# Optimization experiments

Measured on AMD Instinct MI355X. Metric: run time of the kernel, lower is better.

Reference implementation:

```python
import jax, jax.numpy as jnp
import numpy as np

EPS = 1e-5  # torch.nn.LayerNorm default
NUM_HEADS = 8


def _layernorm(x, g, b):
    mu = jnp.mean(x, axis=-1, keepdims=True)
    var = jnp.mean((x - mu) ** 2, axis=-1, keepdims=True)
    return (x - mu) * jax.lax.rsqrt(var + EPS) * g + b


def setup_inputs() -> dict:
    key = jax.random.key(0)
    ks = jax.random.split(key, 8)
    B, S, D = 4, 2048, 512
    scale = 0.02
    return {
        'x': jax.random.normal(ks[0], (B, S, D), dtype=jnp.float32),
        'gene_types': jax.random.randint(ks[1], (B, S), 0, 2),
        'tf_g': jnp.ones((D,), jnp.float32), 'tf_b': jnp.zeros((D,), jnp.float32),
        'tg_g': jnp.ones((D,), jnp.float32), 'tg_b': jnp.zeros((D,), jnp.float32),
        'in_proj_w': jax.random.normal(ks[2], (3 * D, D), dtype=jnp.float32) * scale,
        'in_proj_b': jnp.zeros((3 * D,), jnp.float32),
        'out_proj_w': jax.random.normal(ks[3], (D, D), dtype=jnp.float32) * scale,
        'out_proj_b': jnp.zeros((D,), jnp.float32),
        'w1': jax.random.normal(ks[4], (D // 2, D), dtype=jnp.float32) * scale,
        'b1': jnp.zeros((D // 2,), jnp.float32),
        'w2': jax.random.normal(ks[5], (1, D // 2), dtype=jnp.float32) * scale,
        'b2': jnp.zeros((1,), jnp.float32),
    }


def reference(x, gene_types, tf_g, tf_b, tg_g, tg_b,
              in_proj_w, in_proj_b, out_proj_w, out_proj_b,
              w1, b1, w2, b2):
    B, S, D = x.shape
    H = NUM_HEADS
    HD = D // H
    # --- vectorized per-token conditional LayerNorm (gene_type 0 -> tf, 1 -> target, else passthrough) ---
    gt = gene_types[..., None]
    xn = jnp.where(gt == 0, _layernorm(x, tf_g, tf_b),
                   jnp.where(gt == 1, _layernorm(x, tg_g, tg_b), x))
    # --- multi-head self-attention (torch MultiheadAttention, batch_first) ---
    qkv = xn @ in_proj_w.T + in_proj_b            # [B,S,3D]
    q, k, v = jnp.split(qkv, 3, axis=-1)
    to_heads = lambda t: t.reshape(B, S, H, HD).transpose(0, 2, 1, 3)  # [B,H,S,HD]
    q, k, v = to_heads(q), to_heads(k), to_heads(v)
    scores = jnp.einsum('bhqd,bhkd->bhqk', q, k) / jnp.sqrt(jnp.float32(HD))
    attn = jax.nn.softmax(scores, axis=-1)
    o = jnp.einsum('bhqk,bhkd->bhqd', attn, v)
    o = o.transpose(0, 2, 1, 3).reshape(B, S, D)
    o = o @ out_proj_w.T + out_proj_b
    xr = xn + o                                    # residual
    # --- regulatory strength gate: Linear -> SiLU -> Linear -> Sigmoid ---
    h = jax.nn.silu(xr @ w1.T + b1)                # [B,S,D/2]
    strength = jax.nn.sigmoid(h @ w2.T + b2)       # [B,S,1]
    return xr * strength
```

## Files before the change

kernel.cpp:

```cpp
#include <hip/hip_runtime.h>

typedef __bf16 bf16;
typedef __bf16 bf16x4_t __attribute__((ext_vector_type(4)));
typedef __bf16 bf16x8_t __attribute__((ext_vector_type(8)));
typedef float f32x4_t __attribute__((ext_vector_type(4)));

#define MFMA16(a, b, c) __builtin_amdgcn_mfma_f32_16x16x32_bf16(a, b, c, 0, 0, 0)

__global__ __launch_bounds__(256) void castln_k(const float* __restrict__ Wqkv,
                                                const float* __restrict__ Wout,
                                                const float* __restrict__ W1,
                                                bf16* __restrict__ wq,
                                                bf16* __restrict__ wo,
                                                bf16* __restrict__ w1b,
                                                const float* __restrict__ x,
                                                const int* __restrict__ gt,
                                                const float* __restrict__ tfg,
                                                const float* __restrict__ tfb,
                                                const float* __restrict__ tgg,
                                                const float* __restrict__ tgb,
                                                bf16* __restrict__ xn) {
    if (blockIdx.x < 4608) {
        int i = blockIdx.x * 256 + threadIdx.x;
        if (i < 786432) wq[i] = (bf16)Wqkv[i];
        else if (i < 1048576) wo[i - 786432] = (bf16)Wout[i - 786432];
        else if (i < 1179648) w1b[i - 1048576] = (bf16)W1[i - 1048576];
        return;
    }
    int wid = threadIdx.x >> 6, lane = threadIdx.x & 63;
    int t = (blockIdx.x - 4608) * 4 + wid;
    const float4* xr = (const float4*)(x + (size_t)t * 512);
    float4 a = xr[lane * 2], b = xr[lane * 2 + 1];
    float s = (a.x + a.y) + (a.z + a.w) + (b.x + b.y) + (b.z + b.w);
    float sq = a.x * a.x + a.y * a.y + a.z * a.z + a.w * a.w +
               b.x * b.x + b.y * b.y + b.z * b.z + b.w * b.w;
    for (int m = 1; m < 64; m <<= 1) {
        s += __shfl_xor(s, m, 64);
        sq += __shfl_xor(sq, m, 64);
    }
    float mean = s * (1.f / 512.f);
    float var = fmaxf(sq * (1.f / 512.f) - mean * mean, 0.f);
    float rstd = rsqrtf(var + 1e-5f);
    int g = gt[t];
    float4 o0, o1;
    if (g < 2) {
        const float4* gp = (const float4*)(g ? tgg : tfg);
        const float4* bp = (const float4*)(g ? tgb : tfb);
        float4 g0 = gp[lane * 2], g1 = gp[lane * 2 + 1];
        float4 b0 = bp[lane * 2], b1 = bp[lane * 2 + 1];
        o0.x = (a.x - mean) * rstd * g0.x + b0.x;
        o0.y = (a.y - mean) * rstd * g0.y + b0.y;
        o0.z = (a.z - mean) * rstd * g0.z + b0.z;
        o0.w = (a.w - mean) * rstd * g0.w + b0.w;
        o1.x = (b.x - mean) * rstd * g1.x + b1.x;
        o1.y = (b.y - mean) * rstd * g1.y + b1.y;
        o1.z = (b.z - mean) * rstd * g1.z + b1.z;
        o1.w = (b.w - mean) * rstd * g1.w + b1.w;
    } else {
        o0 = a; o1 = b;
    }
    bf16* xo = xn + (size_t)t * 512 + lane * 8;
    bf16x4_t p0, p1;
    p0[0] = (bf16)o0.x; p0[1] = (bf16)o0.y; p0[2] = (bf16)o0.z; p0[3] = (bf16)o0.w;
    p1[0] = (bf16)o1.x; p1[1] = (bf16)o1.y; p1[2] = (bf16)o1.z; p1[3] = (bf16)o1.w;
    *(bf16x4_t*)xo = p0;
    *(bf16x4_t*)(xo + 4) = p1;
}

__global__ __launch_bounds__(256) void gemmqkv_k(const bf16* __restrict__ A,
                                                 const bf16* __restrict__ B,
                                                 const float* __restrict__ bias,
                                                 bf16* __restrict__ q,
                                                 bf16* __restrict__ kk,
                                                 bf16* __restrict__ vv) {
    int m0 = blockIdx.x * 128, n0 = blockIdx.y * 128;
    int tid = threadIdx.x;
    int lane = tid & 63, w = tid >> 6;
    int quad = lane >> 4, l15 = lane & 15;
    int wm = (w >> 1) * 64, wn = (w & 1) * 64;
    __shared__ bf16 As[128 * 72];
    __shared__ bf16 Bs[128 * 72];
    f32x4_t acc[4][4] = {};
    int srow = tid >> 3, ssub = tid & 7;
    const bf16* Ab = A + (size_t)(m0 + srow) * 512 + ssub * 8;
    const bf16* Bb = B + (size_t)(n0 + srow) * 512 + ssub * 8;
    uint4 pa[4], pb[4];
    auto gload = [&](int s) {
        int k0 = s * 64;
#pragma unroll
        for (int i = 0; i < 4; ++i) {
            pa[i] = *(const uint4*)(Ab + (size_t)(i * 32) * 512 + k0);
            pb[i] = *(const uint4*)(Bb + (size_t)(i * 32) * 512 + k0);
        }
    };
    auto sstore = [&]() {
#pragma unroll
        for (int i = 0; i < 4; ++i) {
            *(uint4*)&As[(i * 32 + srow) * 72 + ssub * 8] = pa[i];
            *(uint4*)&Bs[(i * 32 + srow) * 72 + ssub * 8] = pb[i];
        }
    };
    gload(0);
    sstore();
    for (int s = 0; s < 8; ++s) {
        __syncthreads();
        if (s < 7) gload(s + 1);
#pragma unroll
        for (int ks = 0; ks < 2; ++ks) {
            bf16x8_t af[4], bfr[4];
            int koff = ks * 32 + quad * 8;
#pragma unroll
            for (int mt = 0; mt < 4; ++mt)
                af[mt] = *(const bf16x8_t*)&As[(wm + mt * 16 + l15) * 72 + koff];
#pragma unroll
            for (int nt = 0; nt < 4; ++nt)
                bfr[nt] = *(const bf16x8_t*)&Bs[(wn + nt * 16 + l15) * 72 + koff];
#pragma unroll
            for (int mt = 0; mt < 4; ++mt)
#pragma unroll
                for (int nt = 0; nt < 4; ++nt)
                    acc[mt][nt] = MFMA16(af[mt], bfr[nt], acc[mt][nt]);
        }
        __syncthreads();
        if (s < 7) sstore();
    }
#pragma unroll
    for (int mt = 0; mt < 4; ++mt) {
#pragma unroll
        for (int nt = 0; nt < 4; ++nt) {
            int gcol = n0 + wn + nt * 16 + l15;
            float bcol = bias[gcol];
#pragma unroll
            for (int r = 0; r < 4; ++r) {
                int grow = m0 + wm + mt * 16 + quad * 4 + r;
                float v = acc[mt][nt][r] + bcol;
                int which = gcol >> 9;
                int d = gcol & 511;
                int hh = d >> 6, hd = d & 63;
                int b = grow >> 11, ssi = grow & 2047;
                size_t bh = (size_t)(b * 8 + hh);
                size_t idx = (bh * 2048 + ssi) * 64 + hd;
                if (which == 0) {
                    q[idx] = (bf16)(v * 0.180336880111f);
                } else if (which == 1) {
                    kk[idx] = (bf16)v;
                } else {
                    vv[idx] = (bf16)v;
                }
            }
        }
    }
}

__global__ __launch_bounds__(256) void vtrans_k(const bf16* __restrict__ v,
                                                bf16* __restrict__ vt) {
    int bh = blockIdx.y;
    int s0 = blockIdx.x * 64;
    __shared__ bf16 Ls[64][72];
    int tid = threadIdx.x;
    int row = tid >> 2, seg = tid & 3;
    const bf16* vb = v + ((size_t)bh * 2048 + s0 + row) * 64 + seg * 16;
    *(uint4*)&Ls[row][seg * 16] = *(const uint4*)vb;
    *(uint4*)&Ls[row][seg * 16 + 8] = *(const uint4*)(vb + 8);
    __syncthreads();
    bf16 tmp[16];
#pragma unroll
    for (int i = 0; i < 16; ++i) tmp[i] = Ls[seg * 16 + i][row];
    bf16* dst = vt + ((size_t)bh * 64 + row) * 2048 + s0 + seg * 16;
    *(uint4*)dst = *(uint4*)&tmp[0];
    *(uint4*)(dst + 8) = *(uint4*)&tmp[8];
}

__global__ __launch_bounds__(256) void attn_k(const bf16* __restrict__ q,
                                              const bf16* __restrict__ k,
                                              const bf16* __restrict__ vt,
                                              bf16* __restrict__ pO,
                                              float* __restrict__ pL) {
    int bh = blockIdx.y;
    int q0 = blockIdx.x * 128;
    int sz = blockIdx.z;
    int kt0 = sz * 16;
    int tid = threadIdx.x;
    int lane = tid & 63, w = tid >> 6;
    int quad = lane >> 4, l15 = lane & 15;
    __shared__ bf16 Ks[64 * 72];
    __shared__ bf16 Vs[64 * 72];
    __shared__ bf16 Ps[128 * 72];
    const bf16* qb = q + (size_t)bh * 2048 * 64;
    const bf16* kb = k + (size_t)bh * 2048 * 64;
    const bf16* vb = vt + (size_t)bh * 64 * 2048;
    bf16x8_t qf[2][2];
#pragma unroll
    for (int mt = 0; mt < 2; ++mt)
#pragma unroll
        for (int ks = 0; ks < 2; ++ks)
            qf[mt][ks] = *(const bf16x8_t*)(qb + (size_t)(q0 + w * 32 + mt * 16 + l15) * 64 + ks * 32 + quad * 8);
    bf16x8_t ones8;
#pragma unroll
    for (int i = 0; i < 8; ++i) ones8[i] = (bf16)1.0f;
    f32x4_t oacc[2][4] = {};
    f32x4_t lacc[2] = {};
    int srow = tid >> 3, ssub = tid & 7;
    uint4 pk[2], pw[2];
    auto gload = [&](int kt) {
        int kbase = kt * 64;
#pragma unroll
        for (int i = 0; i < 2; ++i) {
            int row = i * 32 + srow;
            pk[i] = *(const uint4*)(kb + (size_t)(kbase + row) * 64 + ssub * 8);
            pw[i] = *(const uint4*)(vb + (size_t)row * 2048 + kbase + ssub * 8);
        }
    };
    auto sstore = [&]() {
#pragma unroll
        for (int i = 0; i < 2; ++i) {
            int row = i * 32 + srow;
            *(uint4*)&Ks[row * 72 + ssub * 8] = pk[i];
            *(uint4*)&Vs[row * 72 + ssub * 8] = pw[i];
        }
    };
    gload(kt0);
    for (int kt = kt0; kt < kt0 + 16; ++kt) {
        __syncthreads();
        sstore();
        __syncthreads();
        if (kt + 1 < kt0 + 16) gload(kt + 1);
        f32x4_t sacc[2][4] = {};
#pragma unroll
        for (int ks = 0; ks < 2; ++ks) {
            int koff = ks * 32 + quad * 8;
            bf16x8_t kf[4];
#pragma unroll
            for (int nt = 0; nt < 4; ++nt)
                kf[nt] = *(const bf16x8_t*)&Ks[(nt * 16 + l15) * 72 + koff];
#pragma unroll
            for (int mt = 0; mt < 2; ++mt)
#pragma unroll
                for (int nt = 0; nt < 4; ++nt)
                    sacc[mt][nt] = MFMA16(qf[mt][ks], kf[nt], sacc[mt][nt]);
        }
#pragma unroll
        for (int mt = 0; mt < 2; ++mt)
#pragma unroll
            for (int nt = 0; nt < 4; ++nt)
#pragma unroll
                for (int r = 0; r < 4; ++r)
                    Ps[(w * 32 + mt * 16 + quad * 4 + r) * 72 + nt * 16 + l15] = (bf16)exp2f(sacc[mt][nt][r]);
#pragma unroll
        for (int ks = 0; ks < 2; ++ks) {
            int koff = ks * 32 + quad * 8;
            bf16x8_t pf[2], vf[4];
#pragma unroll
            for (int mt = 0; mt < 2; ++mt)
                pf[mt] = *(const bf16x8_t*)&Ps[(w * 32 + mt * 16 + l15) * 72 + koff];
#pragma unroll
            for (int nt = 0; nt < 4; ++nt)
                vf[nt] = *(const bf16x8_t*)&Vs[(nt * 16 + l15) * 72 + koff];
#pragma unroll
            for (int mt = 0; mt < 2; ++mt) {
#pragma unroll
                for (int nt = 0; nt < 4; ++nt)
                    oacc[mt][nt] = MFMA16(pf[mt], vf[nt], oacc[mt][nt]);
                lacc[mt] = MFMA16(pf[mt], ones8, lacc[mt]);
            }
        }
    }
    size_t obase = ((size_t)(sz * 32 + bh) * 2048 + q0);
#pragma unroll
    for (int mt = 0; mt < 2; ++mt)
#pragma unroll
        for (int r = 0; r < 4; ++r) {
            int row = w * 32 + mt * 16 + quad * 4 + r;
#pragma unroll
            for (int nt = 0; nt < 4; ++nt)
                pO[(obase + row) * 64 + nt * 16 + l15] = (bf16)oacc[mt][nt][r];
            if (l15 == 0) pL[obase + row] = lacc[mt][r];
        }
}

__global__ __launch_bounds__(256) void gemmo_k(const bf16* __restrict__ pO,
                                               const float* __restrict__ pL,
                                               const bf16* __restrict__ B,
                                               const float* __restrict__ bias,
                                               const bf16* __restrict__ xn,
                                               bf16* __restrict__ xrb,
                                               float* __restrict__ xrf) {
    int m0 = blockIdx.x * 128, n0 = blockIdx.y * 128;
    int tid = threadIdx.x;
    int lane = tid & 63, w = tid >> 6;
    int quad = lane >> 4, l15 = lane & 15;
    int wm = (w >> 1) * 64, wn = (w & 1) * 64;
    __shared__ bf16 As[128 * 72];
    __shared__ bf16 Bs[128 * 72];
    f32x4_t acc[4][4] = {};
    int srow = tid >> 3, ssub = tid & 7;
    const bf16* Bb = B + (size_t)(n0 + srow) * 512 + ssub * 8;
    bf16x8_t pa[4];
    uint4 pb[4];
    auto gload = [&](int s) {
        int k0 = s * 64;
#pragma unroll
        for (int i = 0; i < 4; ++i) {
            int t = m0 + i * 32 + srow;
            int b = t >> 11, ssi = t & 2047;
            size_t r0 = ((size_t)(b * 8 + s)) * 2048 + ssi;
            size_t r1 = ((size_t)(32 + b * 8 + s)) * 2048 + ssi;
            float inv = 1.f / (pL[r0] + pL[r1]);
            bf16x8_t a0 = *(const bf16x8_t*)(pO + r0 * 64 + ssub * 8);
            bf16x8_t a1 = *(const bf16x8_t*)(pO + r1 * 64 + ssub * 8);
            bf16x8_t c;
#pragma unroll
            for (int j = 0; j < 8; ++j) c[j] = (bf16)(((float)a0[j] + (float)a1[j]) * inv);
            pa[i] = c;
            pb[i] = *(const uint4*)(Bb + (size_t)(i * 32) * 512 + k0);
        }
    };
    auto sstore = [&]() {
#pragma unroll
        for (int i = 0; i < 4; ++i) {
            *(bf16x8_t*)&As[(i * 32 + srow) * 72 + ssub * 8] = pa[i];
            *(uint4*)&Bs[(i * 32 + srow) * 72 + ssub * 8] = pb[i];
        }
    };
    gload(0);
    sstore();
    for (int s = 0; s < 8; ++s) {
        __syncthreads();
        if (s < 7) gload(s + 1);
#pragma unroll
        for (int ks = 0; ks < 2; ++ks) {
            bf16x8_t af[4], bfr[4];
            int koff = ks * 32 + quad * 8;
#pragma unroll
            for (int mt = 0; mt < 4; ++mt)
                af[mt] = *(const bf16x8_t*)&As[(wm + mt * 16 + l15) * 72 + koff];
#pragma unroll
            for (int nt = 0; nt < 4; ++nt)
                bfr[nt] = *(const bf16x8_t*)&Bs[(wn + nt * 16 + l15) * 72 + koff];
#pragma unroll
            for (int mt = 0; mt < 4; ++mt)
#pragma unroll
                for (int nt = 0; nt < 4; ++nt)
                    acc[mt][nt] = MFMA16(af[mt], bfr[nt], acc[mt][nt]);
        }
        __syncthreads();
        if (s < 7) sstore();
    }
#pragma unroll
    for (int mt = 0; mt < 4; ++mt) {
#pragma unroll
        for (int nt = 0; nt < 4; ++nt) {
            int gcol = n0 + wn + nt * 16 + l15;
            float bcol = bias[gcol];
#pragma unroll
            for (int r = 0; r < 4; ++r) {
                int grow = m0 + wm + mt * 16 + quad * 4 + r;
                size_t idx = (size_t)grow * 512 + gcol;
                float xv = acc[mt][nt][r] + bcol + (float)xn[idx];
                xrf[idx] = xv;
                xrb[idx] = (bf16)xv;
            }
        }
    }
}

__global__ __launch_bounds__(256) void mlp_k(const bf16* __restrict__ A,
                                             const bf16* __restrict__ B,
                                             const float* __restrict__ b1,
                                             const float* __restrict__ w2,
                                             const float* __restrict__ b2,
                                             const float* __restrict__ xrf,
                                             float* __restrict__ out) {
    int m0 = blockIdx.x * 32;
    int tid = threadIdx.x;
    int lane = tid & 63, w = tid >> 6;
    int quad = lane >> 4, l15 = lane & 15;
    int wn = w * 64;
    __shared__ bf16 As[32 * 72];
    __shared__ bf16 Bs[256 * 72];
    __shared__ float red[4][32];
    __shared__ float st[32];
    f32x4_t acc[2][4] = {};
    int srow = tid >> 3, ssub = tid & 7;
    uint4 pa, pb[8];
    auto gload = [&](int s) {
        int k0 = s * 64;
        pa = *(const uint4*)(A + (size_t)(m0 + srow) * 512 + ssub * 8 + k0);
#pragma unroll
        for (int i = 0; i < 8; ++i)
            pb[i] = *(const uint4*)(B + (size_t)(i * 32 + srow) * 512 + ssub * 8 + k0);
    };
    auto sstore = [&]() {
        *(uint4*)&As[srow * 72 + ssub * 8] = pa;
#pragma unroll
        for (int i = 0; i < 8; ++i)
            *(uint4*)&Bs[(i * 32 + srow) * 72 + ssub * 8] = pb[i];
    };
    gload(0);
    sstore();
    for (int s = 0; s < 8; ++s) {
        __syncthreads();
        if (s < 7) gload(s + 1);
#pragma unroll
        for (int ks = 0; ks < 2; ++ks) {
            int koff = ks * 32 + quad * 8;
            bf16x8_t af[2], bfr[4];
#pragma unroll
            for (int mt = 0; mt < 2; ++mt)
                af[mt] = *(const bf16x8_t*)&As[(mt * 16 + l15) * 72 + koff];
#pragma unroll
            for (int nt = 0; nt < 4; ++nt)
                bfr[nt] = *(const bf16x8_t*)&Bs[(wn + nt * 16 + l15) * 72 + koff];
#pragma unroll
            for (int mt = 0; mt < 2; ++mt)
#pragma unroll
                for (int nt = 0; nt < 4; ++nt)
                    acc[mt][nt] = MFMA16(af[mt], bfr[nt], acc[mt][nt]);
        }
        __syncthreads();
        if (s < 7) sstore();
    }
    f32x4_t ds[2] = {};
#pragma unroll
    for (int mt = 0; mt < 2; ++mt)
#pragma unroll
        for (int nt = 0; nt < 4; ++nt) {
            int gcol = wn + nt * 16 + l15;
            float bb = b1[gcol], ww = w2[gcol];
#pragma unroll
            for (int r = 0; r < 4; ++r) {
                float v = acc[mt][nt][r] + bb;
                float sv = v / (1.f + __expf(-v));
                ds[mt][r] += sv * ww;
            }
        }
#pragma unroll
    for (int m = 1; m < 16; m <<= 1)
#pragma unroll
        for (int mt = 0; mt < 2; ++mt)
#pragma unroll
            for (int r = 0; r < 4; ++r) ds[mt][r] += __shfl_xor(ds[mt][r], m, 64);
    if (l15 == 0) {
#pragma unroll
        for (int mt = 0; mt < 2; ++mt)
#pragma unroll
            for (int r = 0; r < 4; ++r) red[w][mt * 16 + quad * 4 + r] = ds[mt][r];
    }
    __syncthreads();
    if (tid < 32) {
        float d = red[0][tid] + red[1][tid] + red[2][tid] + red[3][tid] + b2[0];
        st[tid] = 1.f / (1.f + __expf(-d));
    }
    __syncthreads();
    int row = tid >> 3, seg = tid & 7;
    float sr = st[row];
    const float4* x4 = (const float4*)(xrf + (size_t)(m0 + row) * 512);
    float4* o4 = (float4*)(out + (size_t)(m0 + row) * 512);
#pragma unroll
    for (int jj = 0; jj < 16; ++jj) {
        float4 xv = x4[jj * 8 + seg];
        float4 ov;
        ov.x = xv.x * sr; ov.y = xv.y * sr; ov.z = xv.z * sr; ov.w = xv.w * sr;
        o4[jj * 8 + seg] = ov;
    }
}

extern "C" void kernel_launch(void* const* d_in, const int* in_sizes, int n_in,
                              void* d_out, int out_size, void* d_ws, size_t ws_size,
                              hipStream_t stream) {
    const float* x    = (const float*)d_in[0];
    const int*   gt   = (const int*)d_in[1];
    const float* tfg  = (const float*)d_in[2];
    const float* tfb  = (const float*)d_in[3];
    const float* tgg  = (const float*)d_in[4];
    const float* tgb  = (const float*)d_in[5];
    const float* Wqkv = (const float*)d_in[6];
    const float* bqkv = (const float*)d_in[7];
    const float* Wout = (const float*)d_in[8];
    const float* bout = (const float*)d_in[9];
    const float* W1   = (const float*)d_in[10];
    const float* b1   = (const float*)d_in[11];
    const float* w2   = (const float*)d_in[12];
    const float* b2   = (const float*)d_in[13];
    float* out = (float*)d_out;
    char* ws = (char*)d_ws;

    const size_t MB = 1024 * 1024;
    bf16*  wq  = (bf16*)(ws + 0);
    bf16*  wo  = (bf16*)(ws + 1536 * 512 * 2);
    bf16*  w1b = (bf16*)(ws + (1536 + 512) * 512 * 2);
    float* pL  = (float*)(ws + 2304 * 512 * 2);
    bf16*  xn  = (bf16*)(ws + 4 * MB);
    bf16*  q   = (bf16*)(ws + 12 * MB);
    bf16*  xrb = (bf16*)(ws + 12 * MB);
    bf16*  kk  = (bf16*)(ws + 20 * MB);
    bf16*  vv  = (bf16*)(ws + 28 * MB);
    bf16*  vt  = (bf16*)(ws + 36 * MB);
    float* xrf = (float*)(ws + 28 * MB);
    bf16*  pO  = (bf16*)(ws + 44 * MB);

    castln_k<<<6656, 256, 0, stream>>>(Wqkv, Wout, W1, wq, wo, w1b,
                                       x, gt, tfg, tfb, tgg, tgb, xn);
    gemmqkv_k<<<dim3(64, 12), 256, 0, stream>>>(xn, wq, bqkv, q, kk, vv);
    vtrans_k<<<dim3(32, 32), 256, 0, stream>>>(vv, vt);
    attn_k<<<dim3(16, 32, 2), 256, 0, stream>>>(q, kk, vt, pO, pL);
    gemmo_k<<<dim3(64, 4), 256, 0, stream>>>(pO, pL, wo, bout, xn, xrb, xrf);
    mlp_k<<<256, 256, 0, stream>>>(xrb, w1b, b1, w2, b2, xrf, out);
    (void)in_sizes; (void)n_in; (void)out_size; (void)ws_size;
}
```

Baseline: 331.7 us.

## Transpose attention MFMA operands for vectorized P/O stores; drop bf16 residual copy

The attention kernel swaps the MFMA operand order (K·Q and V·P instead of Q·K and P·V), so each lane holds four consecutive key or head-dim values. P tiles and the output partials can then be written as 4-wide bf16 vectors instead of scalar stores. Separately, the output-projection kernel stops writing a bf16 copy of the residual, and the MLP kernel reads the fp32 residual and converts it to bf16 while loading. This saves one global write, at the cost of twice the bytes read in the MLP A-operand load.

```diff
diff --git a/kernel.cpp b/kernel.cpp
--- a/kernel.cpp
+++ b/kernel.cpp
@@ -191,10 +191,10 @@
     const bf16* vb = vt + (size_t)bh * 64 * 2048;
     bf16x8_t qf[2][2];
 #pragma unroll
-    for (int mt = 0; mt < 2; ++mt)
+    for (int qt = 0; qt < 2; ++qt)
 #pragma unroll
         for (int ks = 0; ks < 2; ++ks)
-            qf[mt][ks] = *(const bf16x8_t*)(qb + (size_t)(q0 + w * 32 + mt * 16 + l15) * 64 + ks * 32 + quad * 8);
+            qf[qt][ks] = *(const bf16x8_t*)(qb + (size_t)(q0 + w * 32 + qt * 16 + l15) * 64 + ks * 32 + quad * 8);
     bf16x8_t ones8;
 #pragma unroll
     for (int i = 0; i < 8; ++i) ones8[i] = (bf16)1.0f;
@@ -225,7 +225,7 @@
         sstore();
         __syncthreads();
         if (kt + 1 < kt0 + 16) gload(kt + 1);
-        f32x4_t sacc[2][4] = {};
+        f32x4_t sacc[4][2] = {};
 #pragma unroll
         for (int ks = 0; ks < 2; ++ks) {
             int koff = ks * 32 + quad * 8;
@@ -234,48 +234,52 @@
             for (int nt = 0; nt < 4; ++nt)
                 kf[nt] = *(const bf16x8_t*)&Ks[(nt * 16 + l15) * 72 + koff];
 #pragma unroll
-            for (int mt = 0; mt < 2; ++mt)
-#pragma unroll
-                for (int nt = 0; nt < 4; ++nt)
-                    sacc[mt][nt] = MFMA16(qf[mt][ks], kf[nt], sacc[mt][nt]);
-        }
-#pragma unroll
-        for (int mt = 0; mt < 2; ++mt)
-#pragma unroll
             for (int nt = 0; nt < 4; ++nt)
 #pragma unroll
-                for (int r = 0; r < 4; ++r)
-                    Ps[(w * 32 + mt * 16 + quad * 4 + r) * 72 + nt * 16 + l15] = (bf16)exp2f(sacc[mt][nt][r]);
+                for (int qt = 0; qt < 2; ++qt)
+                    sacc[nt][qt] = MFMA16(kf[nt], qf[qt][ks], sacc[nt][qt]);
+        }
+#pragma unroll
+        for (int nt = 0; nt < 4; ++nt)
+#pragma unroll
+            for (int qt = 0; qt < 2; ++qt) {
+                bf16x4_t pv;
+#pragma unroll
+                for (int r = 0; r < 4; ++r) pv[r] = (bf16)exp2f(sacc[nt][qt][r]);
+                *(bf16x4_t*)&Ps[(w * 32 + qt * 16 + l15) * 72 + nt * 16 + quad * 4] = pv;
+            }
 #pragma unroll
         for (int ks = 0; ks < 2; ++ks) {
             int koff = ks * 32 + quad * 8;
-            bf16x8_t pf[2], vf[4];
-#pragma unroll
-            for (int mt = 0; mt < 2; ++mt)
-                pf[mt] = *(const bf16x8_t*)&Ps[(w * 32 + mt * 16 + l15) * 72 + koff];
-#pragma unroll
-            for (int nt = 0; nt < 4; ++nt)
-                vf[nt] = *(const bf16x8_t*)&Vs[(nt * 16 + l15) * 72 + koff];
-#pragma unroll
-            for (int mt = 0; mt < 2; ++mt) {
-#pragma unroll
-                for (int nt = 0; nt < 4; ++nt)
-                    oacc[mt][nt] = MFMA16(pf[mt], vf[nt], oacc[mt][nt]);
-                lacc[mt] = MFMA16(pf[mt], ones8, lacc[mt]);
+            bf16x8_t vf[4], pf[2];
+#pragma unroll
+            for (int dt = 0; dt < 4; ++dt)
+                vf[dt] = *(const bf16x8_t*)&Vs[(dt * 16 + l15) * 72 + koff];
+#pragma unroll
+            for (int qt = 0; qt < 2; ++qt)
+                pf[qt] = *(const bf16x8_t*)&Ps[(w * 32 + qt * 16 + l15) * 72 + koff];
+#pragma unroll
+            for (int qt = 0; qt < 2; ++qt) {
+#pragma unroll
+                for (int dt = 0; dt < 4; ++dt)
+                    oacc[qt][dt] = MFMA16(vf[dt], pf[qt], oacc[qt][dt]);
+                lacc[qt] = MFMA16(ones8, pf[qt], lacc[qt]);
             }
         }
     }
     size_t obase = ((size_t)(sz * 32 + bh) * 2048 + q0);
 #pragma unroll
-    for (int mt = 0; mt < 2; ++mt)
-#pragma unroll
-        for (int r = 0; r < 4; ++r) {
-            int row = w * 32 + mt * 16 + quad * 4 + r;
-#pragma unroll
-            for (int nt = 0; nt < 4; ++nt)
-                pO[(obase + row) * 64 + nt * 16 + l15] = (bf16)oacc[mt][nt][r];
-            if (l15 == 0) pL[obase + row] = lacc[mt][r];
-        }
+    for (int qt = 0; qt < 2; ++qt) {
+        int qq = w * 32 + qt * 16 + l15;
+#pragma unroll
+        for (int dt = 0; dt < 4; ++dt) {
+            bf16x4_t ov;
+#pragma unroll
+            for (int r = 0; r < 4; ++r) ov[r] = (bf16)oacc[qt][dt][r];
+            *(bf16x4_t*)&pO[(obase + qq) * 64 + dt * 16 + quad * 4] = ov;
+        }
+        if (quad == 0) pL[obase + qq] = lacc[qt][0];
+    }
 }
 
 __global__ __launch_bounds__(256) void gemmo_k(const bf16* __restrict__ pO,
@@ -283,7 +287,6 @@
                                                const bf16* __restrict__ B,
                                                const float* __restrict__ bias,
                                                const bf16* __restrict__ xn,
-                                               bf16* __restrict__ xrb,
                                                float* __restrict__ xrf) {
     int m0 = blockIdx.x * 128, n0 = blockIdx.y * 128;
     int tid = threadIdx.x;
@@ -356,16 +359,13 @@
             for (int r = 0; r < 4; ++r) {
                 int grow = m0 + wm + mt * 16 + quad * 4 + r;
                 size_t idx = (size_t)grow * 512 + gcol;
-                float xv = acc[mt][nt][r] + bcol + (float)xn[idx];
-                xrf[idx] = xv;
-                xrb[idx] = (bf16)xv;
+                xrf[idx] = acc[mt][nt][r] + bcol + (float)xn[idx];
             }
         }
     }
 }
 
-__global__ __launch_bounds__(256) void mlp_k(const bf16* __restrict__ A,
-                                             const bf16* __restrict__ B,
+__global__ __launch_bounds__(256) void mlp_k(const bf16* __restrict__ B,
                                              const float* __restrict__ b1,
                                              const float* __restrict__ w2,
                                              const float* __restrict__ b2,
@@ -382,16 +382,21 @@
     __shared__ float st[32];
     f32x4_t acc[2][4] = {};
     int srow = tid >> 3, ssub = tid & 7;
-    uint4 pa, pb[8];
+    bf16x8_t pa;
+    uint4 pb[8];
     auto gload = [&](int s) {
         int k0 = s * 64;
-        pa = *(const uint4*)(A + (size_t)(m0 + srow) * 512 + ssub * 8 + k0);
+        const float* ar = xrf + (size_t)(m0 + srow) * 512 + ssub * 8 + k0;
+        float4 f0 = *(const float4*)ar;
+        float4 f1 = *(const float4*)(ar + 4);
+        pa[0] = (bf16)f0.x; pa[1] = (bf16)f0.y; pa[2] = (bf16)f0.z; pa[3] = (bf16)f0.w;
+        pa[4] = (bf16)f1.x; pa[5] = (bf16)f1.y; pa[6] = (bf16)f1.z; pa[7] = (bf16)f1.w;
 #pragma unroll
         for (int i = 0; i < 8; ++i)
             pb[i] = *(const uint4*)(B + (size_t)(i * 32 + srow) * 512 + ssub * 8 + k0);
     };
     auto sstore = [&]() {
-        *(uint4*)&As[srow * 72 + ssub * 8] = pa;
+        *(bf16x8_t*)&As[srow * 72 + ssub * 8] = pa;
 #pragma unroll
         for (int i = 0; i < 8; ++i)
             *(uint4*)&Bs[(i * 32 + srow) * 72 + ssub * 8] = pb[i];
@@ -492,11 +497,10 @@
     float* pL  = (float*)(ws + 2304 * 512 * 2);
     bf16*  xn  = (bf16*)(ws + 4 * MB);
     bf16*  q   = (bf16*)(ws + 12 * MB);
-    bf16*  xrb = (bf16*)(ws + 12 * MB);
     bf16*  kk  = (bf16*)(ws + 20 * MB);
+    float* xrf = (float*)(ws + 12 * MB);
     bf16*  vv  = (bf16*)(ws + 28 * MB);
     bf16*  vt  = (bf16*)(ws + 36 * MB);
-    float* xrf = (float*)(ws + 28 * MB);
     bf16*  pO  = (bf16*)(ws + 44 * MB);
 
     castln_k<<<6656, 256, 0, stream>>>(Wqkv, Wout, W1, wq, wo, w1b,
@@ -504,7 +508,7 @@
     gemmqkv_k<<<dim3(64, 12), 256, 0, stream>>>(xn, wq, bqkv, q, kk, vv);
     vtrans_k<<<dim3(32, 32), 256, 0, stream>>>(vv, vt);
     attn_k<<<dim3(16, 32, 2), 256, 0, stream>>>(q, kk, vt, pO, pL);
-    gemmo_k<<<dim3(64, 4), 256, 0, stream>>>(pO, pL, wo, bout, xn, xrb, xrf);
-    mlp_k<<<256, 256, 0, stream>>>(xrb, w1b, b1, w2, b2, xrf, out);
+    gemmo_k<<<dim3(64, 4), 256, 0, stream>>>(pO, pL, wo, bout, xn, xrf);
+    mlp_k<<<256, 256, 0, stream>>>(w1b, b1, w2, b2, xrf, out);
     (void)in_sizes; (void)n_in; (void)out_size; (void)ws_size;
 }
```

Measured after the change: 330.6 us. No clear change (-0.3%).

## Fuse V transpose into QKV GEMM epilogue and widen attention key split

Applied to the files above, without the earlier changes.

The QKV GEMM now writes V directly in transposed layout through a shared-memory staging tile, which removes the separate transpose kernel and its extra round trip of V through memory. The attention kernel is templated on the number of key tiles per split and uses a 4-way split when workspace allows, which gives more blocks and more parallelism, at the cost of more partial results to merge in the output projection. The register prefetch pipeline in attention is dropped in favour of direct global-to-LDS loads. The bf16 copy of the residual is removed, and the MLP instead reads the fp32 residual and casts it on load.

```diff
diff --git a/kernel.cpp b/kernel.cpp
--- a/kernel.cpp
+++ b/kernel.cpp
@@ -72,14 +72,15 @@
                                                  const float* __restrict__ bias,
                                                  bf16* __restrict__ q,
                                                  bf16* __restrict__ kk,
-                                                 bf16* __restrict__ vv) {
+                                                 bf16* __restrict__ vt) {
     int m0 = blockIdx.x * 128, n0 = blockIdx.y * 128;
     int tid = threadIdx.x;
     int lane = tid & 63, w = tid >> 6;
     int quad = lane >> 4, l15 = lane & 15;
     int wm = (w >> 1) * 64, wn = (w & 1) * 64;
-    __shared__ bf16 As[128 * 72];
-    __shared__ bf16 Bs[128 * 72];
+    __shared__ bf16 smem[128 * 144];
+    bf16* As = smem;
+    bf16* Bs = smem + 128 * 72;
     f32x4_t acc[4][4] = {};
     int srow = tid >> 3, ssub = tid & 7;
     const bf16* Ab = A + (size_t)(m0 + srow) * 512 + ssub * 8;
@@ -124,53 +125,57 @@
         __syncthreads();
         if (s < 7) sstore();
     }
-#pragma unroll
-    for (int mt = 0; mt < 4; ++mt) {
-#pragma unroll
-        for (int nt = 0; nt < 4; ++nt) {
-            int gcol = n0 + wn + nt * 16 + l15;
-            float bcol = bias[gcol];
-#pragma unroll
-            for (int r = 0; r < 4; ++r) {
-                int grow = m0 + wm + mt * 16 + quad * 4 + r;
-                float v = acc[mt][nt][r] + bcol;
-                int which = gcol >> 9;
-                int d = gcol & 511;
-                int hh = d >> 6, hd = d & 63;
-                int b = grow >> 11, ssi = grow & 2047;
-                size_t bh = (size_t)(b * 8 + hh);
-                size_t idx = (bh * 2048 + ssi) * 64 + hd;
-                if (which == 0) {
-                    q[idx] = (bf16)(v * 0.180336880111f);
-                } else if (which == 1) {
-                    kk[idx] = (bf16)v;
-                } else {
-                    vv[idx] = (bf16)v;
+    if (blockIdx.y < 8) {
+#pragma unroll
+        for (int mt = 0; mt < 4; ++mt) {
+#pragma unroll
+            for (int nt = 0; nt < 4; ++nt) {
+                int gcol = n0 + wn + nt * 16 + l15;
+                float bcol = bias[gcol];
+#pragma unroll
+                for (int r = 0; r < 4; ++r) {
+                    int grow = m0 + wm + mt * 16 + quad * 4 + r;
+                    float v = acc[mt][nt][r] + bcol;
+                    int d = gcol & 511;
+                    int hh = d >> 6, hd = d & 63;
+                    int b = grow >> 11, ssi = grow & 2047;
+                    size_t idx = (((size_t)(b * 8 + hh)) * 2048 + ssi) * 64 + hd;
+                    if (gcol < 512) q[idx] = (bf16)(v * 0.180336880111f);
+                    else kk[idx] = (bf16)v;
                 }
             }
         }
+    } else {
+        __syncthreads();
+#pragma unroll
+        for (int mt = 0; mt < 4; ++mt)
+#pragma unroll
+            for (int nt = 0; nt < 4; ++nt) {
+                int gcol = n0 + wn + nt * 16 + l15;
+                float bcol = bias[gcol];
+#pragma unroll
+                for (int r = 0; r < 4; ++r) {
+                    int tok = wm + mt * 16 + quad * 4 + r;
+                    smem[tok * 136 + wn + nt * 16 + l15] = (bf16)(acc[mt][nt][r] + bcol);
+                }
+            }
+        __syncthreads();
+        int dl = tid >> 1, seg = tid & 1;
+        int d = (n0 - 1024) + dl;
+        int hh = d >> 6, hd = d & 63;
+        int b = m0 >> 11, ssi0 = m0 & 2047;
+        bf16* dst = vt + ((size_t)(b * 8 + hh) * 64 + hd) * 2048 + ssi0 + seg * 64;
+#pragma unroll
+        for (int u = 0; u < 8; ++u) {
+            bf16 tmp[8];
+#pragma unroll
+            for (int j = 0; j < 8; ++j) tmp[j] = smem[(seg * 64 + u * 8 + j) * 136 + dl];
+            *(uint4*)(dst + u * 8) = *(uint4*)tmp;
+        }
     }
 }
 
-__global__ __launch_bounds__(256) void vtrans_k(const bf16* __restrict__ v,
-                                                bf16* __restrict__ vt) {
-    int bh = blockIdx.y;
-    int s0 = blockIdx.x * 64;
-    __shared__ bf16 Ls[64][72];
-    int tid = threadIdx.x;
-    int row = tid >> 2, seg = tid & 3;
-    const bf16* vb = v + ((size_t)bh * 2048 + s0 + row) * 64 + seg * 16;
-    *(uint4*)&Ls[row][seg * 16] = *(const uint4*)vb;
-    *(uint4*)&Ls[row][seg * 16 + 8] = *(const uint4*)(vb + 8);
-    __syncthreads();
-    bf16 tmp[16];
-#pragma unroll
-    for (int i = 0; i < 16; ++i) tmp[i] = Ls[seg * 16 + i][row];
-    bf16* dst = vt + ((size_t)bh * 64 + row) * 2048 + s0 + seg * 16;
-    *(uint4*)dst = *(uint4*)&tmp[0];
-    *(uint4*)(dst + 8) = *(uint4*)&tmp[8];
-}
-
+template <int TILES>
 __global__ __launch_bounds__(256) void attn_k(const bf16* __restrict__ q,
                                               const bf16* __restrict__ k,
                                               const bf16* __restrict__ vt,
@@ -179,7 +184,6 @@
     int bh = blockIdx.y;
     int q0 = blockIdx.x * 128;
     int sz = blockIdx.z;
-    int kt0 = sz * 16;
     int tid = threadIdx.x;
     int lane = tid & 63, w = tid >> 6;
     int quad = lane >> 4, l15 = lane & 15;
@@ -201,38 +205,23 @@
     f32x4_t oacc[2][4] = {};
     f32x4_t lacc[2] = {};
     int srow = tid >> 3, ssub = tid & 7;
-    uint4 pk[2], pw[2];
-    auto gload = [&](int kt) {
+    for (int kt = sz * TILES; kt < sz * TILES + TILES; ++kt) {
         int kbase = kt * 64;
+        __syncthreads();
 #pragma unroll
         for (int i = 0; i < 2; ++i) {
             int row = i * 32 + srow;
-            pk[i] = *(const uint4*)(kb + (size_t)(kbase + row) * 64 + ssub * 8);
-            pw[i] = *(const uint4*)(vb + (size_t)row * 2048 + kbase + ssub * 8);
-        }
-    };
-    auto sstore = [&]() {
-#pragma unroll
-        for (int i = 0; i < 2; ++i) {
-            int row = i * 32 + srow;
-            *(uint4*)&Ks[row * 72 + ssub * 8] = pk[i];
-            *(uint4*)&Vs[row * 72 + ssub * 8] = pw[i];
-        }
-    };
-    gload(kt0);
-    for (int kt = kt0; kt < kt0 + 16; ++kt) {
-        __syncthreads();
-        sstore();
-        __syncthreads();
-        if (kt + 1 < kt0 + 16) gload(kt + 1);
+            *(uint4*)&Ks[row * 72 + ssub * 8] = *(const uint4*)(kb + (size_t)(kbase + row) * 64 + ssub * 8);
+            *(uint4*)&Vs[row * 72 + ssub * 8] = *(const uint4*)(vb + (size_t)row * 2048 + kbase + ssub * 8);
+        }
+        __syncthreads();
         f32x4_t sacc[2][4] = {};
 #pragma unroll
         for (int ks = 0; ks < 2; ++ks) {
+            bf16x8_t kf[4];
             int koff = ks * 32 + quad * 8;
-            bf16x8_t kf[4];
-#pragma unroll
-            for (int nt = 0; nt < 4; ++nt)
-                kf[nt] = *(const bf16x8_t*)&Ks[(nt * 16 + l15) * 72 + koff];
+#pragma unroll
+            for (int nt = 0; nt < 4; ++nt) kf[nt] = *(const bf16x8_t*)&Ks[(nt * 16 + l15) * 72 + koff];
 #pragma unroll
             for (int mt = 0; mt < 2; ++mt)
 #pragma unroll
@@ -251,11 +240,9 @@
             int koff = ks * 32 + quad * 8;
             bf16x8_t pf[2], vf[4];
 #pragma unroll
-            for (int mt = 0; mt < 2; ++mt)
-                pf[mt] = *(const bf16x8_t*)&Ps[(w * 32 + mt * 16 + l15) * 72 + koff];
-#pragma unroll
-            for (int nt = 0; nt < 4; ++nt)
-                vf[nt] = *(const bf16x8_t*)&Vs[(nt * 16 + l15) * 72 + koff];
+            for (int mt = 0; mt < 2; ++mt) pf[mt] = *(const bf16x8_t*)&Ps[(w * 32 + mt * 16 + l15) * 72 + koff];
+#pragma unroll
+            for (int nt = 0; nt < 4; ++nt) vf[nt] = *(const bf16x8_t*)&Vs[(nt * 16 + l15) * 72 + koff];
 #pragma unroll
             for (int mt = 0; mt < 2; ++mt) {
 #pragma unroll
@@ -278,12 +265,12 @@
         }
 }
 
+template <int NSPLIT>
 __global__ __launch_bounds__(256) void gemmo_k(const bf16* __restrict__ pO,
                                                const float* __restrict__ pL,
                                                const bf16* __restrict__ B,
                                                const float* __restrict__ bias,
                                                const bf16* __restrict__ xn,
-                                               bf16* __restrict__ xrb,
                                                float* __restrict__ xrf) {
     int m0 = blockIdx.x * 128, n0 = blockIdx.y * 128;
     int tid = threadIdx.x;
@@ -303,14 +290,20 @@
         for (int i = 0; i < 4; ++i) {
             int t = m0 + i * 32 + srow;
             int b = t >> 11, ssi = t & 2047;
-            size_t r0 = ((size_t)(b * 8 + s)) * 2048 + ssi;
-            size_t r1 = ((size_t)(32 + b * 8 + s)) * 2048 + ssi;
-            float inv = 1.f / (pL[r0] + pL[r1]);
-            bf16x8_t a0 = *(const bf16x8_t*)(pO + r0 * 64 + ssub * 8);
-            bf16x8_t a1 = *(const bf16x8_t*)(pO + r1 * 64 + ssub * 8);
+            float lsum = 0.f;
+            float facc[8] = {};
+#pragma unroll
+            for (int sp = 0; sp < NSPLIT; ++sp) {
+                size_t r = ((size_t)(sp * 32 + b * 8 + s)) * 2048 + ssi;
+                lsum += pL[r];
+                bf16x8_t av = *(const bf16x8_t*)(pO + r * 64 + ssub * 8);
+#pragma unroll
+                for (int j = 0; j < 8; ++j) facc[j] += (float)av[j];
+            }
+            float inv = 1.f / lsum;
             bf16x8_t c;
 #pragma unroll
-            for (int j = 0; j < 8; ++j) c[j] = (bf16)(((float)a0[j] + (float)a1[j]) * inv);
+            for (int j = 0; j < 8; ++j) c[j] = (bf16)(facc[j] * inv);
             pa[i] = c;
             pb[i] = *(const uint4*)(Bb + (size_t)(i * 32) * 512 + k0);
         }
@@ -356,16 +349,13 @@
             for (int r = 0; r < 4; ++r) {
                 int grow = m0 + wm + mt * 16 + quad * 4 + r;
                 size_t idx = (size_t)grow * 512 + gcol;
-                float xv = acc[mt][nt][r] + bcol + (float)xn[idx];
-                xrf[idx] = xv;
-                xrb[idx] = (bf16)xv;
+                xrf[idx] = acc[mt][nt][r] + bcol + (float)xn[idx];
             }
         }
     }
 }
 
-__global__ __launch_bounds__(256) void mlp_k(const bf16* __restrict__ A,
-                                             const bf16* __restrict__ B,
+__global__ __launch_bounds__(256) void mlp_k(const bf16* __restrict__ B,
                                              const float* __restrict__ b1,
                                              const float* __restrict__ w2,
                                              const float* __restrict__ b2,
@@ -382,16 +372,21 @@
     __shared__ float st[32];
     f32x4_t acc[2][4] = {};
     int srow = tid >> 3, ssub = tid & 7;
-    uint4 pa, pb[8];
+    bf16x8_t pa;
+    uint4 pb[8];
     auto gload = [&](int s) {
         int k0 = s * 64;
-        pa = *(const uint4*)(A + (size_t)(m0 + srow) * 512 + ssub * 8 + k0);
+        const float* ar = xrf + (size_t)(m0 + srow) * 512 + ssub * 8 + k0;
+        float4 f0 = *(const float4*)ar;
+        float4 f1 = *(const float4*)(ar + 4);
+        pa[0] = (bf16)f0.x; pa[1] = (bf16)f0.y; pa[2] = (bf16)f0.z; pa[3] = (bf16)f0.w;
+        pa[4] = (bf16)f1.x; pa[5] = (bf16)f1.y; pa[6] = (bf16)f1.z; pa[7] = (bf16)f1.w;
 #pragma unroll
         for (int i = 0; i < 8; ++i)
             pb[i] = *(const uint4*)(B + (size_t)(i * 32 + srow) * 512 + ssub * 8 + k0);
     };
     auto sstore = [&]() {
-        *(uint4*)&As[srow * 72 + ssub * 8] = pa;
+        *(bf16x8_t*)&As[srow * 72 + ssub * 8] = pa;
 #pragma unroll
         for (int i = 0; i < 8; ++i)
             *(uint4*)&Bs[(i * 32 + srow) * 72 + ssub * 8] = pb[i];
@@ -492,19 +487,21 @@
     float* pL  = (float*)(ws + 2304 * 512 * 2);
     bf16*  xn  = (bf16*)(ws + 4 * MB);
     bf16*  q   = (bf16*)(ws + 12 * MB);
-    bf16*  xrb = (bf16*)(ws + 12 * MB);
     bf16*  kk  = (bf16*)(ws + 20 * MB);
-    bf16*  vv  = (bf16*)(ws + 28 * MB);
-    bf16*  vt  = (bf16*)(ws + 36 * MB);
-    float* xrf = (float*)(ws + 28 * MB);
-    bf16*  pO  = (bf16*)(ws + 44 * MB);
+    float* xrf = (float*)(ws + 12 * MB);
+    bf16*  vt  = (bf16*)(ws + 28 * MB);
+    bf16*  pO  = (bf16*)(ws + 36 * MB);
 
     castln_k<<<6656, 256, 0, stream>>>(Wqkv, Wout, W1, wq, wo, w1b,
                                        x, gt, tfg, tfb, tgg, tgb, xn);
-    gemmqkv_k<<<dim3(64, 12), 256, 0, stream>>>(xn, wq, bqkv, q, kk, vv);
-    vtrans_k<<<dim3(32, 32), 256, 0, stream>>>(vv, vt);
-    attn_k<<<dim3(16, 32, 2), 256, 0, stream>>>(q, kk, vt, pO, pL);
-    gemmo_k<<<dim3(64, 4), 256, 0, stream>>>(pO, pL, wo, bout, xn, xrb, xrf);
-    mlp_k<<<256, 256, 0, stream>>>(xrb, w1b, b1, w2, b2, xrf, out);
-    (void)in_sizes; (void)n_in; (void)out_size; (void)ws_size;
+    gemmqkv_k<<<dim3(64, 12), 256, 0, stream>>>(xn, wq, bqkv, q, kk, vt);
+    if (ws_size >= 69 * MB) {
+        attn_k<8><<<dim3(16, 32, 4), 256, 0, stream>>>(q, kk, vt, pO, pL);
+        gemmo_k<4><<<dim3(64, 4), 256, 0, stream>>>(pO, pL, wo, bout, xn, xrf);
+    } else {
+        attn_k<16><<<dim3(16, 32, 2), 256, 0, stream>>>(q, kk, vt, pO, pL);
+        gemmo_k<2><<<dim3(64, 4), 256, 0, stream>>>(pO, pL, wo, bout, xn, xrf);
+    }
+    mlp_k<<<256, 256, 0, stream>>>(w1b, b1, w2, b2, xrf, out);
+    (void)in_sizes; (void)n_in; (void)out_size;
 }
```

Result: faster. 314.9 us (-5.1%).
